# Kernel optimization log

Hardware: AMD Instinct MI355X
Metric: run time of the kernel (lower is better)

## Reference

```python
import jax, jax.numpy as jnp
import numpy as np

B, L, D = 4096, 200, 128
EPS = 1e-12  # Keras l2_normalize epsilon


def _l2_normalize(x):
    # K.l2_normalize: x / sqrt(max(sum(x^2), eps))
    sq = jnp.sum(x * x, axis=-1, keepdims=True)
    return x * jax.lax.rsqrt(jnp.maximum(sq, EPS))


def setup_inputs() -> dict:
    key = jax.random.key(0)
    k1, k2, k3, k4 = jax.random.split(key, 4)
    return {
        "recentTimeRepresentations": jax.random.normal(k1, (B, L, D), dtype=jnp.float32),
        "curTimeRepresentation": jax.random.normal(k2, (B, D), dtype=jnp.float32),
        "recentTimestamps": jax.random.randint(k3, (B, L), 0, 2, dtype=jnp.int32),
        "recentItemEmbeddings": jax.random.normal(k4, (B, L, D), dtype=jnp.float32),
    }


def reference(recentTimeRepresentations, curTimeRepresentation, recentTimestamps, recentItemEmbeddings):
    mask = (recentTimestamps > 0).astype(jnp.float32)  # [B, L]
    cur_n = _l2_normalize(curTimeRepresentation)        # [B, D]
    rec_n = _l2_normalize(recentTimeRepresentations)    # [B, L, D]
    # cosine similarity of current rep vs each history rep
    similarity = jnp.einsum("bd,bld->bl", cur_n, rec_n)  # [B, L]
    masked_similarity = mask * ((similarity + 1.0) * 0.5)  # [B, L]
    # weighted sum of history item embeddings (no softmax)
    userHistoryRepresentation = jnp.einsum("bl,bld->bd", masked_similarity, recentItemEmbeddings)
    return userHistoryRepresentation
```

## Files before the change

kernel.cpp:

```cpp
#include <hip/hip_runtime.h>

#define B_ 4096
#define L_ 200
#define D_ 128

__global__ __launch_bounds__(256, 8) void tahe_kernel(
    const float* __restrict__ rec,
    const float* __restrict__ cur,
    const int*   __restrict__ ts,
    const float* __restrict__ item,
    float*       __restrict__ out)
{
    const int b    = blockIdx.x;
    const int tid  = threadIdx.x;
    const int wave = tid >> 6;
    const int grp  = tid >> 5;
    const int half = (tid >> 5) & 1;
    const int sub  = tid & 31;

    __shared__ int    s_active[L_];
    __shared__ int    s_n;
    __shared__ float4 s_red[4][32];

    if (tid == 0) s_n = 0;
    __syncthreads();

    if (tid < L_) {
        if (ts[b * L_ + tid] > 0) {
            int p = atomicAdd(&s_n, 1);
            s_active[p] = tid;
        }
    }

    const float4 c4 = *(const float4*)(cur + b * D_ + sub * 4);
    float css = c4.x*c4.x + c4.y*c4.y + c4.z*c4.z + c4.w*c4.w;
    #pragma unroll
    for (int m = 1; m <= 16; m <<= 1) css += __shfl_xor(css, m);
    float crs = rsqrtf(fmaxf(css, 1e-12f));
    crs = crs * (1.5f - 0.5f * css * crs * crs);
    float4 cn;
    cn.x = c4.x * crs; cn.y = c4.y * crs; cn.z = c4.z * crs; cn.w = c4.w * crs;

    __syncthreads();
    const int n = s_n;

    const float* recb  = rec  + (size_t)b * (L_ * D_);
    const float* itemb = item + (size_t)b * (L_ * D_);

    float4 acc = make_float4(0.f, 0.f, 0.f, 0.f);

    for (int i = grp; i < n; i += 8) {
        const int l = s_active[i];
        const float4 r4 = *(const float4*)(recb  + l * D_ + sub * 4);
        const float4 t4 = *(const float4*)(itemb + l * D_ + sub * 4);

        float pd = cn.x*r4.x + cn.y*r4.y + cn.z*r4.z + cn.w*r4.w;
        float ps = r4.x*r4.x + r4.y*r4.y + r4.z*r4.z + r4.w*r4.w;
        #pragma unroll
        for (int m = 1; m <= 16; m <<= 1) {
            pd += __shfl_xor(pd, m);
            ps += __shfl_xor(ps, m);
        }
        float rs = rsqrtf(fmaxf(ps, 1e-12f));
        rs = rs * (1.5f - 0.5f * ps * rs * rs);
        const float w = fmaf(pd * rs, 0.5f, 0.5f);

        acc.x = fmaf(w, t4.x, acc.x);
        acc.y = fmaf(w, t4.y, acc.y);
        acc.z = fmaf(w, t4.z, acc.z);
        acc.w = fmaf(w, t4.w, acc.w);
    }

    acc.x += __shfl_xor(acc.x, 32);
    acc.y += __shfl_xor(acc.y, 32);
    acc.z += __shfl_xor(acc.z, 32);
    acc.w += __shfl_xor(acc.w, 32);

    if (half == 0) s_red[wave][sub] = acc;
    __syncthreads();

    if (tid < D_) {
        const float* rf = (const float*)s_red;
        float v = rf[tid] + rf[D_ + tid] + rf[2 * D_ + tid] + rf[3 * D_ + tid];
        out[b * D_ + tid] = v;
    }
}

extern "C" void kernel_launch(void* const* d_in, const int* in_sizes, int n_in,
                              void* d_out, int out_size, void* d_ws, size_t ws_size,
                              hipStream_t stream) {
    const float* rec  = (const float*)d_in[0];
    const float* cur  = (const float*)d_in[1];
    const int*   ts   = (const int*)d_in[2];
    const float* item = (const float*)d_in[3];
    float*       out  = (float*)d_out;
    tahe_kernel<<<B_, 256, 0, stream>>>(rec, cur, ts, item, out);
}
```

Before: 704.4 us.

## Split kernel into similarity-weight phase and weighted item-sum phase

Restructures the per-batch kernel into two phases. First, groups of 8 threads each compute one active row's dot product and norm with a 3-step shuffle reduction and store the weights in shared memory. Second, 32-thread groups stream the item embeddings and accumulate the weighted sum. This removes the 5-step double shuffle reduction on every row and decouples the rec and item loads, at the cost of an extra barrier and a wider 8-way final reduction.

```diff
diff --git a/kernel.cpp b/kernel.cpp
--- a/kernel.cpp
+++ b/kernel.cpp
@@ -11,16 +11,14 @@
     const float* __restrict__ item,
     float*       __restrict__ out)
 {
-    const int b    = blockIdx.x;
-    const int tid  = threadIdx.x;
-    const int wave = tid >> 6;
-    const int grp  = tid >> 5;
-    const int half = (tid >> 5) & 1;
-    const int sub  = tid & 31;
+    const int b   = blockIdx.x;
+    const int tid = threadIdx.x;
 
-    __shared__ int    s_active[L_];
+    __shared__ int    s_act[L_];
+    __shared__ float  s_w[L_];
     __shared__ int    s_n;
-    __shared__ float4 s_red[4][32];
+    __shared__ float  s_cinv;
+    __shared__ float4 s_red[8][32];
 
     if (tid == 0) s_n = 0;
     __syncthreads();
@@ -28,60 +26,85 @@
     if (tid < L_) {
         if (ts[b * L_ + tid] > 0) {
             int p = atomicAdd(&s_n, 1);
-            s_active[p] = tid;
+            s_act[p] = tid;
         }
     }
 
-    const float4 c4 = *(const float4*)(cur + b * D_ + sub * 4);
-    float css = c4.x*c4.x + c4.y*c4.y + c4.z*c4.z + c4.w*c4.w;
-    #pragma unroll
-    for (int m = 1; m <= 16; m <<= 1) css += __shfl_xor(css, m);
-    float crs = rsqrtf(fmaxf(css, 1e-12f));
-    crs = crs * (1.5f - 0.5f * css * crs * crs);
-    float4 cn;
-    cn.x = c4.x * crs; cn.y = c4.y * crs; cn.z = c4.z * crs; cn.w = c4.w * crs;
+    if (tid < 32) {
+        const float4 c4 = *(const float4*)(cur + b * D_ + tid * 4);
+        float ss = c4.x*c4.x + c4.y*c4.y + c4.z*c4.z + c4.w*c4.w;
+        #pragma unroll
+        for (int m = 1; m <= 16; m <<= 1) ss += __shfl_xor(ss, m);
+        if (tid == 0) {
+            float r = rsqrtf(fmaxf(ss, 1e-12f));
+            r = r * (1.5f - 0.5f * ss * r * r);
+            s_cinv = r;
+        }
+    }
+    __syncthreads();
 
-    __syncthreads();
-    const int n = s_n;
-
+    const int   n    = s_n;
+    const float cinv = s_cinv;
     const float* recb  = rec  + (size_t)b * (L_ * D_);
     const float* itemb = item + (size_t)b * (L_ * D_);
 
+    {
+        const int g8 = tid >> 3;
+        const int j  = tid & 7;
+        float4 c[4];
+        #pragma unroll
+        for (int k = 0; k < 4; ++k)
+            c[k] = *(const float4*)(cur + b * D_ + (j + 8 * k) * 4);
+
+        for (int i = g8; i < n; i += 32) {
+            const int l = s_act[i];
+            const float* r = recb + (size_t)l * D_;
+            float pd = 0.f, ps = 0.f;
+            #pragma unroll
+            for (int k = 0; k < 4; ++k) {
+                const float4 r4 = *(const float4*)(r + (j + 8 * k) * 4);
+                pd = fmaf(c[k].x, r4.x, fmaf(c[k].y, r4.y, fmaf(c[k].z, r4.z, fmaf(c[k].w, r4.w, pd))));
+                ps = fmaf(r4.x, r4.x, fmaf(r4.y, r4.y, fmaf(r4.z, r4.z, fmaf(r4.w, r4.w, ps))));
+            }
+            #pragma unroll
+            for (int m = 1; m <= 4; m <<= 1) {
+                pd += __shfl_xor(pd, m);
+                ps += __shfl_xor(ps, m);
+            }
+            if (j == 0) {
+                float rs = rsqrtf(fmaxf(ps, 1e-12f));
+                rs = rs * (1.5f - 0.5f * ps * rs * rs);
+                s_w[i] = fmaf(pd * rs * cinv, 0.5f, 0.5f);
+            }
+        }
+    }
+    __syncthreads();
+
+    const int g   = tid >> 5;
+    const int sub = tid & 31;
     float4 acc = make_float4(0.f, 0.f, 0.f, 0.f);
 
-    for (int i = grp; i < n; i += 8) {
-        const int l = s_active[i];
-        const float4 r4 = *(const float4*)(recb  + l * D_ + sub * 4);
-        const float4 t4 = *(const float4*)(itemb + l * D_ + sub * 4);
-
-        float pd = cn.x*r4.x + cn.y*r4.y + cn.z*r4.z + cn.w*r4.w;
-        float ps = r4.x*r4.x + r4.y*r4.y + r4.z*r4.z + r4.w*r4.w;
-        #pragma unroll
-        for (int m = 1; m <= 16; m <<= 1) {
-            pd += __shfl_xor(pd, m);
-            ps += __shfl_xor(ps, m);
-        }
-        float rs = rsqrtf(fmaxf(ps, 1e-12f));
-        rs = rs * (1.5f - 0.5f * ps * rs * rs);
-        const float w = fmaf(pd * rs, 0.5f, 0.5f);
-
+    for (int i = g; i < n; i += 8) {
+        const int   l = s_act[i];
+        const float w = s_w[i];
+        const float4 t4 = *(const float4*)(itemb + (size_t)l * D_ + sub * 4);
         acc.x = fmaf(w, t4.x, acc.x);
         acc.y = fmaf(w, t4.y, acc.y);
         acc.z = fmaf(w, t4.z, acc.z);
         acc.w = fmaf(w, t4.w, acc.w);
     }
 
-    acc.x += __shfl_xor(acc.x, 32);
-    acc.y += __shfl_xor(acc.y, 32);
-    acc.z += __shfl_xor(acc.z, 32);
-    acc.w += __shfl_xor(acc.w, 32);
-
-    if (half == 0) s_red[wave][sub] = acc;
+    s_red[g][sub] = acc;
     __syncthreads();
 
     if (tid < D_) {
-        const float* rf = (const float*)s_red;
-        float v = rf[tid] + rf[D_ + tid] + rf[2 * D_ + tid] + rf[3 * D_ + tid];
+        const int chunk = tid >> 2, comp = tid & 3;
+        float v = 0.f;
+        #pragma unroll
+        for (int gg = 0; gg < 8; ++gg) {
+            const float* rf = (const float*)&s_red[gg][chunk];
+            v += rf[comp];
+        }
         out[b * D_ + tid] = v;
     }
 }
```

New measurement: 701.5 us. Within noise of the previous version (-0.4%).
